# Performance work log

Measured on AMD Instinct MI355X. Metric: run time of the kernel, lower is better.

The kernel has to match this reference:

```python
import jax, jax.numpy as jnp
import numpy as np

CP = (96, 96, 96)      # control-point grid size (D, H, W)
NSTEPS = 7             # VecInt int_steps
N_TP = 4               # timepoints
# all ordered pairs i<j: tid 'ti_to_tj' -> ref=i, flo=j  (K = 6)
REF_IDX = np.array([0, 0, 0, 1, 1, 2])
FLO_IDX = np.array([1, 2, 3, 2, 3, 3])


def _make_grid(shape):
    axes = [jnp.arange(s, dtype=jnp.float32) for s in shape]
    return jnp.stack(jnp.meshgrid(*axes, indexing='ij'), axis=0)  # (3, D, H, W)

GRID = _make_grid(CP)


def trilinear_sample(vol, coords):
    """Sample channels-first volume at absolute voxel coordinates.

    vol:    (C, D, H, W) field values
    coords: (3, D, H, W) absolute (i, j, k) voxel coordinates
    returns (C, D, H, W); border (clamp) handling at edges.
    """
    D, H, W = vol.shape[1:]
    x, y, z = coords[0], coords[1], coords[2]
    x0f = jnp.floor(x); y0f = jnp.floor(y); z0f = jnp.floor(z)
    fx = x - x0f; fy = y - y0f; fz = z - z0f
    x0 = jnp.clip(x0f.astype(jnp.int32), 0, D - 1)
    x1 = jnp.clip(x0 + 1, 0, D - 1)
    y0 = jnp.clip(y0f.astype(jnp.int32), 0, H - 1)
    y1 = jnp.clip(y0 + 1, 0, H - 1)
    z0 = jnp.clip(z0f.astype(jnp.int32), 0, W - 1)
    z1 = jnp.clip(z0 + 1, 0, W - 1)

    c000 = vol[:, x0, y0, z0]; c001 = vol[:, x0, y0, z1]
    c010 = vol[:, x0, y1, z0]; c011 = vol[:, x0, y1, z1]
    c100 = vol[:, x1, y0, z0]; c101 = vol[:, x1, y0, z1]
    c110 = vol[:, x1, y1, z0]; c111 = vol[:, x1, y1, z1]

    c00 = c000 * (1 - fz) + c001 * fz
    c01 = c010 * (1 - fz) + c011 * fz
    c10 = c100 * (1 - fz) + c101 * fz
    c11 = c110 * (1 - fz) + c111 * fz
    c0 = c00 * (1 - fy) + c01 * fy
    c1 = c10 * (1 - fy) + c11 * fy
    return c0 * (1 - fx) + c1 * fx


def vecint(v):
    """Scaling-and-squaring integration of stationary velocity field v: (3,D,H,W)."""
    v = v * (1.0 / 2.0 ** NSTEPS)
    for _ in range(NSTEPS):
        v = v + trilinear_sample(v, GRID + v)
    return v


def compose_fields(f1, f2):
    """(grid + f1 + f2(grid + f1)) - grid, fields (3,D,H,W)."""
    return f1 + trilinear_sample(f2, GRID + f1)


def setup_inputs() -> dict:
    key = jax.random.key(0)
    k1, k2 = jax.random.split(key)
    T = jax.random.normal(k1, (N_TP, 3) + CP, dtype=jnp.float32)
    R = jax.random.normal(k2, CP + (3, len(REF_IDX)), dtype=jnp.float32)
    return {"T": T, "R": R}


def reference(T, R):
    # integrate +/- velocity for every timepoint once (same math as per-pair calls)
    F_pos = jax.vmap(vecint)(T)           # (N, 3, D, H, W) = integrate(T[t])
    F_neg = jax.vmap(vecint)(-T)          # (N, 3, D, H, W) = integrate(-T[t])
    ref = jnp.asarray(REF_IDX)
    flo = jnp.asarray(FLO_IDX)
    # R_hat[k] = compose(integrate(-T[ref_k]), integrate(T[flo_k]))  -> (K,3,D,H,W)
    R_hat = jax.vmap(compose_fields)(F_neg[ref], F_pos[flo])
    # original permutes R_hat to (D,H,W,3,K); equivalently permute R the other way
    residue = R_hat - jnp.transpose(R, (4, 3, 0, 1, 2))  # (K,3,D,H,W)
    # l1 cost: sum_k,x sqrt(sum_c residue^2)
    loss = jnp.sum(jnp.sqrt(jnp.sum(residue ** 2, axis=1)))
    return loss
```

## Files before the change

kernel.cpp:

```cpp
#include <hip/hip_runtime.h>
#include <hip/hip_fp16.h>

#define NV    884736
#define NB    3456
#define DIM   96
#define DIM2  9216
#define NF    6
#define SLACK 32


union H4 { uint2 u; __half2 h2[2]; };
union H8 { uint4 u; __half2 h2[4]; };

struct F3 { float x, y, z; };

__device__ __forceinline__ F3 lerp3(F3 a, F3 b, float t, float omt) {
    F3 r;
    r.x = a.x * omt + b.x * t;
    r.y = a.y * omt + b.y * t;
    r.z = a.z * omt + b.z * t;
    return r;
}

__device__ __forceinline__ uint2 pack_h4(float x, float y, float z) {
    H4 v;
    v.h2[0] = __floats2half2_rn(x, y);
    v.h2[1] = __floats2half2_rn(z, 0.0f);
    return v.u;
}

__device__ __forceinline__ F3 unpack_h4(uint2 raw) {
    H4 v; v.u = raw;
    float2 xy = __half22float2(v.h2[0]);
    float2 zp = __half22float2(v.h2[1]);
    F3 r; r.x = xy.x; r.y = xy.y; r.z = zp.x;
    return r;
}

struct TriIdx { int idx[4]; float fx, fy, fz; };

__device__ __forceinline__ TriIdx tri_prep(float x, float y, float z) {
    TriIdx t;
    float xf = floorf(x), yf = floorf(y), zf = floorf(z);
    t.fx = x - xf; t.fy = y - yf;
    float fz = z - zf;
    int x0 = (int)xf; x0 = x0 < 0 ? 0 : (x0 > DIM - 1 ? DIM - 1 : x0);
    int y0 = (int)yf; y0 = y0 < 0 ? 0 : (y0 > DIM - 1 ? DIM - 1 : y0);
    int z0 = (int)zf; z0 = z0 < 0 ? 0 : (z0 > DIM - 1 ? DIM - 1 : z0);
    int x1 = x0 + 1; if (x1 > DIM - 1) x1 = DIM - 1;
    int y1 = y0 + 1; if (y1 > DIM - 1) y1 = DIM - 1;
    t.fz = (z0 < DIM - 1) ? fz : 0.0f;
    int X0 = x0 * DIM2, X1 = x1 * DIM2;
    int Y0 = y0 * DIM,  Y1 = y1 * DIM;
    t.idx[0] = X0 + Y0 + z0;
    t.idx[1] = X0 + Y1 + z0;
    t.idx[2] = X1 + Y0 + z0;
    t.idx[3] = X1 + Y1 + z0;
    return t;
}

__device__ __forceinline__ void tri_gather(const uint2* __restrict__ f,
                                           const TriIdx& t, H8 c[4]) {
    #pragma unroll
    for (int q = 0; q < 4; q++)
        c[q].u = *(const uint4*)(f + t.idx[q]);
}

__device__ __forceinline__ F3 tri_combine(const TriIdx& t, const H8 c[4]) {
    float gz = 1.0f - t.fz, gy = 1.0f - t.fy, gx = 1.0f - t.fx;
    F3 pz[4];
    #pragma unroll
    for (int q = 0; q < 4; q++) {
        float2 xy0 = __half22float2(c[q].h2[0]);
        float2 z0p = __half22float2(c[q].h2[1]);
        float2 xy1 = __half22float2(c[q].h2[2]);
        float2 z1p = __half22float2(c[q].h2[3]);
        F3 lo; lo.x = xy0.x; lo.y = xy0.y; lo.z = z0p.x;
        F3 hi; hi.x = xy1.x; hi.y = xy1.y; hi.z = z1p.x;
        pz[q] = lerp3(lo, hi, t.fz, gz);
    }
    F3 c0 = lerp3(pz[0], pz[1], t.fy, gy);
    F3 c1 = lerp3(pz[2], pz[3], t.fy, gy);
    return lerp3(c0, c1, t.fx, gx);
}

__global__ __launch_bounds__(256) void init_kernel(const float* __restrict__ T,
                                                   uint2* __restrict__ bufA,
                                                   uint2* __restrict__ bufB,
                                                   float* __restrict__ out) {
    int t = blockIdx.y;
    int l = blockIdx.x * 256 + threadIdx.x;
    if (t == 0 && l == 0) out[0] = 0.0f;
    if (t == 0 && l < SLACK) {
        bufA[(size_t)NF * NV + l] = make_uint2(0u, 0u);
        bufB[(size_t)NF * NV + l] = make_uint2(0u, 0u);
    }
    const float inv = 1.0f / 128.0f;
    float vx = T[(size_t)(t * 3 + 0) * NV + l] * inv;
    float vy = T[(size_t)(t * 3 + 1) * NV + l] * inv;
    float vz = T[(size_t)(t * 3 + 2) * NV + l] * inv;
    if (t >= 1) bufA[(size_t)(t - 1) * NV + l] = pack_h4( vx,  vy,  vz);
    if (t <= 2) bufA[(size_t)(t + 3) * NV + l] = pack_h4(-vx, -vy, -vz);
}

#define STEP_VB   NB
#define STEP_W    (STEP_VB * NF)
#define STEP_CHK  (STEP_W / 8)
__global__ __launch_bounds__(256) void step_kernel(const uint2* __restrict__ src,
                                                   uint2* __restrict__ dst) {
    int b   = blockIdx.x;
    int w   = (b & 7) * STEP_CHK + (b >> 3);
    int f   = w / STEP_VB;
    int vb  = w - f * STEP_VB;
    const uint2* __restrict__ s = src + (size_t)f * NV;
    uint2*       __restrict__ d = dst + (size_t)f * NV;

    int l   = vb * 256 + threadIdx.x;
    int i   = l / DIM2;
    int rem = l - i * DIM2;
    int j   = rem / DIM;
    int k   = rem - j * DIM;

    F3 v = unpack_h4(s[l]);
    TriIdx t = tri_prep((float)i + v.x, (float)j + v.y, (float)k + v.z);
    H8 c[4];
    tri_gather(s, t, c);
    F3 smp = tri_combine(t, c);
    d[l] = pack_h4(v.x + smp.x, v.y + smp.y, v.z + smp.z);
}

__global__ __launch_bounds__(256) void loss_kernel(const uint2* __restrict__ fields,
                                                   const float* __restrict__ R,
                                                   float* __restrict__ out) {
    __shared__ float rlds[4 * 1152];
    int b = blockIdx.x;
    int vb = (b & 7) * (NB / 8) + (b >> 3);
    int l = vb * 256 + threadIdx.x;
    int lane = threadIdx.x & 63;
    int wid  = threadIdx.x >> 6;

    {
        const float4* Rw = (const float4*)(R + ((size_t)vb * 256 + wid * 64) * 18);
        float4* lw = (float4*)(rlds + wid * 1152);
        #pragma unroll
        for (int q = 0; q < 5; q++) {
            int idx = q * 64 + lane;
            if (idx < 288) lw[idx] = Rw[idx];
        }
    }
    float* myR = rlds + wid * 1152 + lane * 18;

    int k = l % DIM;
    int j = (l / DIM) % DIM;
    int i = l / DIM2;
    float fi = (float)i, fj = (float)j, fk = (float)k;

    F3 f1c[3];
    #pragma unroll
    for (int r = 0; r < 3; r++)
        f1c[r] = unpack_h4(fields[(size_t)(3 + r) * NV + l]);

    const int REFI[6] = {0, 0, 0, 1, 1, 2};
    const int FLOF[6] = {0, 1, 2, 1, 2, 2};

    float acc = 0.0f;
    #pragma unroll
    for (int p = 0; p < 6; p += 2) {
        F3 f1a = f1c[REFI[p]];
        F3 f1b = f1c[REFI[p + 1]];
        const uint2* __restrict__ f2a = fields + (size_t)FLOF[p]     * NV;
        const uint2* __restrict__ f2b = fields + (size_t)FLOF[p + 1] * NV;
        TriIdx ta = tri_prep(fi + f1a.x, fj + f1a.y, fk + f1a.z);
        TriIdx tb = tri_prep(fi + f1b.x, fj + f1b.y, fk + f1b.z);
        H8 ca[4], cb[4];
        tri_gather(f2a, ta, ca);
        tri_gather(f2b, tb, cb);
        float2 rx2 = *(const float2*)(myR + 0 * 6 + p);
        float2 ry2 = *(const float2*)(myR + 1 * 6 + p);
        float2 rz2 = *(const float2*)(myR + 2 * 6 + p);
        F3 sa = tri_combine(ta, ca);
        F3 sb = tri_combine(tb, cb);
        float rx = f1a.x + sa.x - rx2.x;
        float ry = f1a.y + sa.y - ry2.x;
        float rz = f1a.z + sa.z - rz2.x;
        acc += sqrtf(rx * rx + ry * ry + rz * rz);
        rx = f1b.x + sb.x - rx2.y;
        ry = f1b.y + sb.y - ry2.y;
        rz = f1b.z + sb.z - rz2.y;
        acc += sqrtf(rx * rx + ry * ry + rz * rz);
    }

    __shared__ float wsum[4];
    #pragma unroll
    for (int off = 32; off > 0; off >>= 1)
        acc += __shfl_down(acc, off, 64);
    if (lane == 0) wsum[wid] = acc;
    __syncthreads();
    if (threadIdx.x == 0) {
        float s = wsum[0] + wsum[1] + wsum[2] + wsum[3];
        atomicAdd(out, s);
    }
}

extern "C" void kernel_launch(void* const* d_in, const int* in_sizes, int n_in,
                              void* d_out, int out_size, void* d_ws, size_t ws_size,
                              hipStream_t stream) {
    const float* T = (const float*)d_in[0];
    const float* R = (const float*)d_in[1];
    float* out = (float*)d_out;

    uint2* bufA = (uint2*)d_ws;
    uint2* bufB = bufA + (size_t)NF * NV + SLACK;

    dim3 blk(256);
    init_kernel<<<dim3(NB, 4), blk, 0, stream>>>(T, bufA, bufB, out);

    uint2* src = bufA;
    uint2* dst = bufB;
    for (int s = 0; s < 7; s++) {
        step_kernel<<<STEP_W, blk, 0, stream>>>(src, dst);
        uint2* tmp = src; src = dst; dst = tmp;
    }
    loss_kernel<<<NB, blk, 0, stream>>>(src, R, out);
}
```

Baseline: 349.6 us.

## Split loss kernel across pair groups and use nontemporal stores in step kernel

```diff
diff --git a/kernel.cpp b/kernel.cpp
--- a/kernel.cpp
+++ b/kernel.cpp
@@ -27,6 +27,12 @@
     v.h2[0] = __floats2half2_rn(x, y);
     v.h2[1] = __floats2half2_rn(z, 0.0f);
     return v.u;
+}
+
+__device__ __forceinline__ unsigned long long pack_h4_u64(float x, float y, float z) {
+    union { uint2 u2; unsigned long long u64; } cvt;
+    cvt.u2 = pack_h4(x, y, z);
+    return cvt.u64;
 }
 
 __device__ __forceinline__ F3 unpack_h4(uint2 raw) {
@@ -126,71 +132,59 @@
     H8 c[4];
     tri_gather(s, t, c);
     F3 smp = tri_combine(t, c);
-    d[l] = pack_h4(v.x + smp.x, v.y + smp.y, v.z + smp.z);
-}
-
+    __builtin_nontemporal_store(pack_h4_u64(v.x + smp.x, v.y + smp.y, v.z + smp.z),
+                                (unsigned long long*)&d[l]);
+}
+
+#define NBL3 (NB * 3)
+#define LCHK (NBL3 / 8)
 __global__ __launch_bounds__(256) void loss_kernel(const uint2* __restrict__ fields,
                                                    const float* __restrict__ R,
                                                    float* __restrict__ out) {
-    __shared__ float rlds[4 * 1152];
-    int b = blockIdx.x;
-    int vb = (b & 7) * (NB / 8) + (b >> 3);
-    int l = vb * 256 + threadIdx.x;
-    int lane = threadIdx.x & 63;
-    int wid  = threadIdx.x >> 6;
-
-    {
-        const float4* Rw = (const float4*)(R + ((size_t)vb * 256 + wid * 64) * 18);
-        float4* lw = (float4*)(rlds + wid * 1152);
-        #pragma unroll
-        for (int q = 0; q < 5; q++) {
-            int idx = q * 64 + lane;
-            if (idx < 288) lw[idx] = Rw[idx];
-        }
-    }
-    float* myR = rlds + wid * 1152 + lane * 18;
-
+    int b  = blockIdx.x;
+    int w  = (b & 7) * LCHK + (b >> 3);
+    int vb = w / 3;
+    int pp = w - vb * 3;
+    int l  = vb * 256 + threadIdx.x;
     int k = l % DIM;
     int j = (l / DIM) % DIM;
     int i = l / DIM2;
     float fi = (float)i, fj = (float)j, fk = (float)k;
 
-    F3 f1c[3];
-    #pragma unroll
-    for (int r = 0; r < 3; r++)
-        f1c[r] = unpack_h4(fields[(size_t)(3 + r) * NV + l]);
-
-    const int REFI[6] = {0, 0, 0, 1, 1, 2};
-    const int FLOF[6] = {0, 1, 2, 1, 2, 2};
-
-    float acc = 0.0f;
-    #pragma unroll
-    for (int p = 0; p < 6; p += 2) {
-        F3 f1a = f1c[REFI[p]];
-        F3 f1b = f1c[REFI[p + 1]];
-        const uint2* __restrict__ f2a = fields + (size_t)FLOF[p]     * NV;
-        const uint2* __restrict__ f2b = fields + (size_t)FLOF[p + 1] * NV;
-        TriIdx ta = tri_prep(fi + f1a.x, fj + f1a.y, fk + f1a.z);
-        TriIdx tb = tri_prep(fi + f1b.x, fj + f1b.y, fk + f1b.z);
-        H8 ca[4], cb[4];
-        tri_gather(f2a, ta, ca);
-        tri_gather(f2b, tb, cb);
-        float2 rx2 = *(const float2*)(myR + 0 * 6 + p);
-        float2 ry2 = *(const float2*)(myR + 1 * 6 + p);
-        float2 rz2 = *(const float2*)(myR + 2 * 6 + p);
-        F3 sa = tri_combine(ta, ca);
-        F3 sb = tri_combine(tb, cb);
-        float rx = f1a.x + sa.x - rx2.x;
-        float ry = f1a.y + sa.y - ry2.x;
-        float rz = f1a.z + sa.z - rz2.x;
-        acc += sqrtf(rx * rx + ry * ry + rz * rz);
-        rx = f1b.x + sb.x - rx2.y;
-        ry = f1b.y + sb.y - ry2.y;
-        rz = f1b.z + sb.z - rz2.y;
-        acc += sqrtf(rx * rx + ry * ry + rz * rz);
-    }
+    const int REFA[3] = {0, 0, 1}, REFB[3] = {0, 1, 2};
+    const int FLOA[3] = {0, 2, 2}, FLOB[3] = {1, 1, 2};
+    int p0 = pp * 2;
+
+    const float* Rl = R + (size_t)l * 18 + p0;
+    float2 rx2 = *(const float2*)(Rl + 0 * 6);
+    float2 ry2 = *(const float2*)(Rl + 1 * 6);
+    float2 rz2 = *(const float2*)(Rl + 2 * 6);
+
+    F3 f1a = unpack_h4(fields[(size_t)(3 + REFA[pp]) * NV + l]);
+    F3 f1b = unpack_h4(fields[(size_t)(3 + REFB[pp]) * NV + l]);
+    const uint2* __restrict__ f2a = fields + (size_t)FLOA[pp] * NV;
+    const uint2* __restrict__ f2b = fields + (size_t)FLOB[pp] * NV;
+
+    TriIdx ta = tri_prep(fi + f1a.x, fj + f1a.y, fk + f1a.z);
+    TriIdx tb = tri_prep(fi + f1b.x, fj + f1b.y, fk + f1b.z);
+    H8 ca[4], cb[4];
+    tri_gather(f2a, ta, ca);
+    tri_gather(f2b, tb, cb);
+    F3 sa = tri_combine(ta, ca);
+    F3 sb = tri_combine(tb, cb);
+
+    float rx = f1a.x + sa.x - rx2.x;
+    float ry = f1a.y + sa.y - ry2.x;
+    float rz = f1a.z + sa.z - rz2.x;
+    float acc = sqrtf(rx * rx + ry * ry + rz * rz);
+    rx = f1b.x + sb.x - rx2.y;
+    ry = f1b.y + sb.y - ry2.y;
+    rz = f1b.z + sb.z - rz2.y;
+    acc += sqrtf(rx * rx + ry * ry + rz * rz);
 
     __shared__ float wsum[4];
+    int lane = threadIdx.x & 63;
+    int wid  = threadIdx.x >> 6;
     #pragma unroll
     for (int off = 32; off > 0; off >>= 1)
         acc += __shfl_down(acc, off, 64);
@@ -221,5 +215,5 @@
         step_kernel<<<STEP_W, blk, 0, stream>>>(src, dst);
         uint2* tmp = src; src = dst; dst = tmp;
     }
-    loss_kernel<<<NB, blk, 0, stream>>>(src, R, out);
-}
+    loss_kernel<<<NBL3, blk, 0, stream>>>(src, R, out);
+}
```

After: 475.9 us. 36.1% more time.
